# Performance work log

Hardware: AMD Instinct MI355X
Metric: run time of the kernel (lower is better)

The kernel has to match this reference:

```python
import jax, jax.numpy as jnp
import numpy as np
from jax import lax

B, H, W = 8, 64, 64
D_IN, D_OUT, HEADS = 288, 576, 8
WIN, QS = 16, 2
MLP_H, BOT, NEXP = 4 * D_OUT, 32, 2
HEAD_DIM = D_OUT // HEADS


def _ln(x, g, b, eps=1e-6):
    m = jnp.mean(x, axis=-1, keepdims=True)
    v = jnp.var(x, axis=-1, keepdims=True)
    return (x - m) * lax.rsqrt(v + eps) * g + b


def _max_pool2(x):  # NHWC 2x2 max pool, stride 2
    return lax.reduce_window(x, -jnp.inf, lax.max, (1, 2, 2, 1), (1, 2, 2, 1), 'VALID')


def setup_inputs():
    key = jax.random.key(0)
    ks = iter(jax.random.split(key, 16))
    s = 0.02
    p = {}
    p['rgb'] = jax.random.normal(next(ks), (B, H, W, D_IN), jnp.float32)
    p['depth'] = jax.random.normal(next(ks), (B, H, W, D_IN), jnp.float32)
    p['norm1_g'] = jnp.ones((D_IN,), jnp.float32)
    p['norm1_b'] = jnp.zeros((D_IN,), jnp.float32)
    p['proj_w'] = jax.random.normal(next(ks), (D_IN, D_OUT), jnp.float32) * s
    p['proj_b'] = jnp.zeros((D_OUT,), jnp.float32)
    p['qkv_w'] = jax.random.normal(next(ks), (D_IN, 3 * D_OUT), jnp.float32) * s
    p['qkv_b'] = jnp.zeros((3 * D_OUT,), jnp.float32)
    p['attn_proj_w'] = jax.random.normal(next(ks), (D_OUT, D_OUT), jnp.float32) * s
    p['attn_proj_b'] = jnp.zeros((D_OUT,), jnp.float32)
    p['norm2_g'] = jnp.ones((D_OUT,), jnp.float32)
    p['norm2_b'] = jnp.zeros((D_OUT,), jnp.float32)
    p['mlp_w1'] = jax.random.normal(next(ks), (D_OUT, MLP_H), jnp.float32) * s
    p['mlp_b1'] = jnp.zeros((MLP_H,), jnp.float32)
    p['mlp_w2'] = jax.random.normal(next(ks), (MLP_H, D_OUT), jnp.float32) * s
    p['mlp_b2'] = jnp.zeros((D_OUT,), jnp.float32)
    # per-stream (rgb=0, depth=1) MoE adapters: 2 experts, bottleneck 32
    p['ad_gate_w'] = jax.random.normal(next(ks), (2, D_OUT, NEXP), jnp.float32) * s
    p['ad_gate_b'] = jnp.zeros((2, NEXP), jnp.float32)
    p['ad_down_w'] = jax.random.normal(next(ks), (2, NEXP, D_OUT, BOT), jnp.float32) * s
    p['ad_down_b'] = jnp.zeros((2, NEXP, BOT), jnp.float32)
    p['ad_up_w'] = jax.random.normal(next(ks), (2, NEXP, BOT, D_OUT), jnp.float32) * s
    p['ad_up_b'] = jnp.zeros((2, NEXP, D_OUT), jnp.float32)
    return p


def reference(rgb, depth, norm1_g, norm1_b, proj_w, proj_b, qkv_w, qkv_b,
              attn_proj_w, attn_proj_b, norm2_g, norm2_b,
              mlp_w1, mlp_b1, mlp_w2, mlp_b2,
              ad_gate_w, ad_gate_b, ad_down_w, ad_down_b, ad_up_w, ad_up_b):
    nW = H // WIN  # 4 windows per side (64 divisible by 16, no padding)
    w2 = WIN // QS  # pooled window side = 8

    def adapter(x, si):
        gate = jax.nn.softmax(x @ ad_gate_w[si] + ad_gate_b[si], axis=-1)  # [B,h,w,E]
        h = jax.nn.gelu(jnp.einsum('bhwd,edr->bhwer', x, ad_down_w[si]) + ad_down_b[si])
        y = jnp.einsum('bhwer,erd->bhwed', h, ad_up_w[si]) + ad_up_b[si]
        return 0.5 * jnp.sum(gate[..., None] * y, axis=-2)

    def stream(x, si):
        xn = _ln(x, norm1_g, norm1_b)
        # dim changes -> shortcut = do_pool(proj(norm1(x)))
        shortcut = _max_pool2(xn @ proj_w + proj_b)  # [B,32,32,576]
        xw = xn.reshape(B, nW, WIN, nW, WIN, D_IN).transpose(0, 1, 3, 2, 4, 5)
        xw = xw.reshape(B * nW * nW, WIN, WIN, D_IN)
        Bw = xw.shape[0]
        qkv = (xw.reshape(Bw, WIN * WIN, D_IN) @ qkv_w + qkv_b)
        qkv = qkv.reshape(Bw, WIN * WIN, 3, HEADS, HEAD_DIM)
        q, k, v = qkv[:, :, 0], qkv[:, :, 1], qkv[:, :, 2]
        # q-pool (2x2 max) inside each window
        q = _max_pool2(q.reshape(Bw, WIN, WIN, D_OUT)).reshape(Bw, w2 * w2, HEADS, HEAD_DIM)
        scale = 1.0 / np.sqrt(HEAD_DIM).astype(np.float32)
        attn = jax.nn.softmax(jnp.einsum('bqhd,bkhd->bhqk', q, k) * scale, axis=-1)
        o = jnp.einsum('bhqk,bkhd->bqhd', attn, v).reshape(Bw, w2, w2, D_OUT)
        o = o @ attn_proj_w + attn_proj_b
        # unpartition with pooled window size into 32x32
        o = o.reshape(B, nW, nW, w2, w2, D_OUT).transpose(0, 1, 3, 2, 4, 5)
        o = o.reshape(B, nW * w2, nW * w2, D_OUT)
        x = shortcut + o
        h = _ln(x, norm2_g, norm2_b)
        mlp = jax.nn.gelu(h @ mlp_w1 + mlp_b1) @ mlp_w2 + mlp_b2
        return x + mlp + adapter(x, si)

    return jnp.stack([stream(rgb, 0), stream(depth, 1)])  # [2,B,32,32,576]
```

## Files before the change

kernel.cpp:

```cpp
#include <hip/hip_runtime.h>
#include <cstdint>
#include <math.h>
#include <type_traits>

typedef __bf16 bf16_t;
typedef __bf16 bf16x8 __attribute__((ext_vector_type(8)));
typedef float f32x4 __attribute__((ext_vector_type(4)));
typedef uint32_t u32x4 __attribute__((ext_vector_type(4)));
typedef uint32_t u32x2 __attribute__((ext_vector_type(2)));

#define DI __device__ __forceinline__

DI float bflo(uint32_t u){ return __builtin_bit_cast(float, (uint32_t)(u << 16)); }
DI float bfhi(uint32_t u){ return __builtin_bit_cast(float, (uint32_t)(u & 0xffff0000u)); }
DI uint16_t f2bf(float f){ bf16_t h = (bf16_t)f; return __builtin_bit_cast(uint16_t, h); }
DI uint32_t pk2(float a, float b){ return (uint32_t)f2bf(a) | ((uint32_t)f2bf(b) << 16); }
DI float geluf(float x){
  float t = x * x;
  float p = fmaf(t, 0.0356774081f, 0.7978845608f);
  float e = __expf(-2.0f * x * p);
  return x * __builtin_amdgcn_rcpf(1.0f + e);
}

#if defined(__has_builtin)
#if __has_builtin(__builtin_amdgcn_global_load_lds)
#define USE_GLLDS 1
#endif
#endif

#if USE_GLLDS
DI void gload_lds16(const void* g, void* l){
  __builtin_amdgcn_global_load_lds((__attribute__((address_space(1))) void*)g,
                                   (__attribute__((address_space(3))) void*)l, 16, 0, 0);
}
#endif

__global__ __launch_bounds__(256) void vtpad_k(uint16_t* __restrict__ vt)
{
  int idx = blockIdx.x * 256 + threadIdx.x;
  int wh = idx >> 11, r = (idx >> 8) & 7, c = idx & 255;
  vt[((size_t)(wh * 80 + 72 + r)) * 256 + c] = 0;
}

__global__ __launch_bounds__(256) void wtrans_k(const float* __restrict__ W, uint16_t* __restrict__ Wt,
                                                int K, int N, int Np, int ldw, int c0)
{
  int idx = blockIdx.x * 256 + threadIdx.x;
  if (idx >= Np * K) return;
  int n = idx / K, k = idx - n * K;
  float v = (n < N) ? W[(size_t)k * ldw + c0 + n] : 0.0f;
  Wt[idx] = f2bf(v);
}

__global__ __launch_bounds__(256) void mk_m2te_k(const float* __restrict__ w2,
    const float* __restrict__ uw, const float* __restrict__ ub, uint16_t* __restrict__ m2Te)
{
  int idx = blockIdx.x * 256 + threadIdx.x;
  if (idx >= 2 * 640 * 2400) return;
  int si = idx / (640 * 2400);
  int rem = idx - si * 640 * 2400;
  int n = rem / 2400, k = rem - n * 2400;
  float v = 0.0f;
  if (n < 576){
    if (k < 2304) v = w2[(size_t)k * 576 + n];
    else if (k < 2368){
      int e = (k - 2304) >> 5, r = (k - 2304) & 31;
      v = uw[((size_t)(si * 2 + e) * 32 + r) * 576 + n];
    } else if (k < 2370){
      v = ub[(size_t)(si * 2 + (k - 2368)) * 576 + n];
    }
  }
  m2Te[idx] = f2bf(v);
}

__global__ __launch_bounds__(256) void mk_adt_k(const float* __restrict__ dwn, const float* __restrict__ gw,
    const float* __restrict__ dbn, const float* __restrict__ gb,
    uint16_t* __restrict__ adT, float* __restrict__ adB)
{
  int idx = blockIdx.x * 256 + threadIdx.x;
  if (idx >= 2 * 128 * 576) return;
  int si = idx / (128 * 576);
  int rem = idx - si * 128 * 576;
  int n = rem / 576, k = rem - n * 576;
  float v = 0.0f;
  if (n < 64){
    int e = n >> 5, r = n & 31;
    v = dwn[((size_t)(si * 2 + e) * 576 + k) * 32 + r];
  } else if (n < 66){
    v = gw[(size_t)si * 1152 + k * 2 + (n - 64)];
  }
  adT[idx] = f2bf(v);
  if (k == 0){
    float bv = 0.0f;
    if (n < 64) bv = dbn[si * 64 + (n >> 5) * 32 + (n & 31)];
    else if (n < 66) bv = gb[si * 2 + (n - 64)];
    adB[si * 128 + n] = bv;
  }
}

__global__ __launch_bounds__(256) void mk_pqb_k(const float* __restrict__ pb, const float* __restrict__ qb,
                                                float* __restrict__ o)
{
  int i = blockIdx.x * 256 + threadIdx.x;
  if (i < 1152) o[i] = (i < 576) ? pb[i] : qb[i - 576];
}

template<typename TIN>
__global__ __launch_bounds__(256) void ln_k(const TIN* __restrict__ in0, const int D,
                                            const float* __restrict__ g, const float* __restrict__ bb,
                                            uint16_t* __restrict__ outp)
{
  const int token = blockIdx.x * 4 + (threadIdx.x >> 6);
  const int lane = threadIdx.x & 63;
  const TIN* in = in0 + (size_t)token * D;
  const int nf4 = D >> 2;
  f32x4 v[3];
  float s = 0.f, sq = 0.f;
#pragma unroll
  for (int i = 0; i < 3; ++i){
    const int c = lane + 64 * i;
    if (c < nf4){
      if constexpr (std::is_same<TIN, float>::value){
        v[i] = *(const f32x4*)(in + 4 * c);
      } else {
        u32x2 u = *(const u32x2*)((const uint16_t*)in + 4 * c);
        v[i][0] = bflo(u[0]); v[i][1] = bfhi(u[0]);
        v[i][2] = bflo(u[1]); v[i][3] = bfhi(u[1]);
      }
#pragma unroll
      for (int e = 0; e < 4; ++e){ s += v[i][e]; sq += v[i][e] * v[i][e]; }
    }
  }
#pragma unroll
  for (int off = 32; off; off >>= 1){
    s  += __shfl_xor(s, off);
    sq += __shfl_xor(sq, off);
  }
  const float mean = s / (float)D;
  const float var = sq / (float)D - mean * mean;
  const float inv = rsqrtf(var + 1e-6f);
  uint16_t* orow = outp + (size_t)token * D;
#pragma unroll
  for (int i = 0; i < 3; ++i){
    const int c = lane + 64 * i;
    if (c < nf4){
      float f0 = (v[i][0] - mean) * inv * g[4*c+0] + bb[4*c+0];
      float f1 = (v[i][1] - mean) * inv * g[4*c+1] + bb[4*c+1];
      float f2 = (v[i][2] - mean) * inv * g[4*c+2] + bb[4*c+2];
      float f3 = (v[i][3] - mean) * inv * g[4*c+3] + bb[4*c+3];
      u32x2 pk; pk[0] = pk2(f0, f1); pk[1] = pk2(f2, f3);
      *(u32x2*)(orow + 4 * c) = pk;
    }
  }
}

template<int BM>
DI void gemm_core(const uint16_t* __restrict__ A, const uint16_t* __restrict__ Bt,
                  const int K, char* smem, const int tid, f32x4 (*acc)[4])
{
  constexpr int MI = BM / 32;
  constexpr int ABUF = BM * 64;
  char* A0 = smem;
  char* A1 = smem + ABUF;
  char* B0 = smem + 2 * ABUF;
  char* B1 = smem + 2 * ABUF + 8192;
  const int lane = tid & 63;
  const int wid = tid >> 6;
  const int wm = (wid >> 1) * (BM / 2);
  const int wn = (wid & 1) * 64;
  const int r15 = lane & 15, kh = lane >> 4;
  const int rA0 = tid >> 2, c16 = tid & 3;
  const int kS = ((c16 ^ ((rA0 >> 1) & 3)) << 3);

  auto stage = [&](char* Ad, char* Bd, int t){
    const uint16_t* ga0 = A + (size_t)rA0 * K + t * 32 + kS;
    const uint16_t* gb0 = Bt + (size_t)rA0 * K + t * 32 + kS;
    const uint16_t* gb1 = Bt + (size_t)(rA0 + 64) * K + t * 32 + kS;
#if USE_GLLDS
    gload_lds16(ga0, Ad + tid * 16);
    gload_lds16(gb0, Bd + tid * 16);
    gload_lds16(gb1, Bd + tid * 16 + 4096);
    if constexpr (BM == 128){
      const uint16_t* ga1 = A + (size_t)(rA0 + 64) * K + t * 32 + kS;
      gload_lds16(ga1, Ad + tid * 16 + 4096);
    }
#else
    *(u32x4*)(Ad + tid * 16)        = *(const u32x4*)ga0;
    *(u32x4*)(Bd + tid * 16)        = *(const u32x4*)gb0;
    *(u32x4*)(Bd + tid * 16 + 4096) = *(const u32x4*)gb1;
    if constexpr (BM == 128){
      const uint16_t* ga1 = A + (size_t)(rA0 + 64) * K + t * 32 + kS;
      *(u32x4*)(Ad + tid * 16 + 4096) = *(const u32x4*)ga1;
    }
#endif
  };

  stage(A0, B0, 0);
  __syncthreads();
  const int nt = K >> 5;
  for (int t = 0; t < nt; ++t){
    char* Ac = (t & 1) ? A1 : A0;
    char* Bc = (t & 1) ? B1 : B0;
    if (t + 1 < nt) stage((t & 1) ? A0 : A1, (t & 1) ? B0 : B1, t + 1);
    bf16x8 af[MI], bfv[4];
#pragma unroll
    for (int i = 0; i < MI; ++i){
      int rowA = wm + i * 16 + r15;
      af[i] = *(const bf16x8*)(Ac + rowA * 64 + ((kh ^ ((rowA >> 1) & 3)) << 4));
    }
#pragma unroll
    for (int j = 0; j < 4; ++j){
      int rowB = wn + j * 16 + r15;
      bfv[j] = *(const bf16x8*)(Bc + rowB * 64 + ((kh ^ ((rowB >> 1) & 3)) << 4));
    }
#pragma unroll
    for (int i = 0; i < MI; ++i)
#pragma unroll
      for (int j = 0; j < 4; ++j)
        acc[i][j] = __builtin_amdgcn_mfma_f32_16x16x32_bf16(af[i], bfv[j], acc[i][j], 0, 0, 0);
    __syncthreads();
  }
}

__global__ __launch_bounds__(256) void gemm_pkv_k(
    const uint16_t* __restrict__ xn, const uint16_t* __restrict__ pqT, const uint16_t* __restrict__ kvT,
    const float* __restrict__ pqB, const float* __restrict__ kvB,
    uint16_t* __restrict__ sc, uint16_t* __restrict__ qp,
    uint16_t* __restrict__ kb, uint16_t* __restrict__ vt)
{
  __shared__ __align__(16) char smem[34816];
  const int tid = threadIdx.x;
  const int m0 = blockIdx.x * 128;
  const int y = blockIdx.y;
  const bool pool = (y < 9);
  const int n0 = pool ? y * 128 : (y - 9) * 128;
  const uint16_t* Bt = (pool ? pqT : kvT) + (size_t)n0 * 288;
  f32x4 acc[4][4] = {};
  gemm_core<128>(xn + (size_t)m0 * 288, Bt, 288, smem, tid, acc);

  const int lane = tid & 63, wid = tid >> 6;
  const int wm = (wid >> 1) * 64, wn = (wid & 1) * 64;
  const int r15 = lane & 15, kh = lane >> 4;

  if (pool){
    uint16_t* Cp = (uint16_t*)smem;
#pragma unroll
    for (int i = 0; i < 4; ++i)
#pragma unroll
      for (int j = 0; j < 4; ++j)
#pragma unroll
        for (int tt = 0; tt < 4; ++tt){
          int rr2 = wm + i * 16 + kh * 4 + tt;
          int cc = wn + j * 16 + r15;
          Cp[rr2 * 136 + cc] = f2bf(acc[i][j][tt]);
        }
    __syncthreads();
    const int orow0 = m0 >> 2;
#pragma unroll
    for (int e2 = 0; e2 < 16; ++e2){
      int idx = tid + 256 * e2;
      int X = idx >> 7, c = idx & 127;
      int gn = n0 + c;
      float v0 = bflo(Cp[(2 * X) * 136 + c]);
      float v1 = bflo(Cp[(2 * X + 1) * 136 + c]);
      float v2 = bflo(Cp[(64 + 2 * X) * 136 + c]);
      float v3 = bflo(Cp[(65 + 2 * X) * 136 + c]);
      float v = fmaxf(fmaxf(v0, v1), fmaxf(v2, v3)) + pqB[gn];
      if (gn < 576)
        sc[(size_t)(orow0 + X) * 576 + gn] = f2bf(v);
      else
        qp[(size_t)(orow0 + X) * 576 + (gn - 576)] = f2bf(v);
    }
  } else {
    int coln[4]; float bcol[4];
#pragma unroll
    for (int j = 0; j < 4; ++j){
      coln[j] = n0 + wn + j * 16 + r15;
      bcol[j] = kvB[coln[j]];
    }
#pragma unroll
    for (int i = 0; i < 4; ++i)
#pragma unroll
      for (int tt = 0; tt < 4; ++tt){
        const int gm = m0 + wm + i * 16 + kh * 4 + tt;
#pragma unroll
        for (int j = 0; j < 4; ++j){
          float v = acc[i][j][tt] + bcol[j];
          int n = coln[j];
          if (n < 576){
            kb[(size_t)gm * 576 + n] = f2bf(v);
          } else {
            int d = n - 576;
            int hh = d / 72, dd = d - hh * 72;
            int bimg = gm >> 12, yy = (gm >> 6) & 63, xx = gm & 63;
            int w = bimg * 16 + (yy >> 4) * 4 + (xx >> 4);
            int kl = (yy & 15) * 16 + (xx & 15);
            vt[((size_t)(w * 8 + hh) * 80 + dd) * 256 + kl] = f2bf(v);
          }
        }
      }
  }
}

__global__ __launch_bounds__(256) void gemm_add1_k(
    const uint16_t* __restrict__ ob, const uint16_t* __restrict__ aT, const float* __restrict__ bias,
    const uint16_t* __restrict__ sc, uint16_t* __restrict__ x2b)
{
  __shared__ __align__(16) char smem[32768];
  const int tid = threadIdx.x;
  const int m0 = blockIdx.x * 128;
  const int n0 = blockIdx.y * 128;
  f32x4 acc[4][4] = {};
  gemm_core<128>(ob + (size_t)m0 * 576, aT + (size_t)n0 * 576, 576, smem, tid, acc);

  const int lane = tid & 63, wid = tid >> 6;
  const int wm = (wid >> 1) * 64, wn = (wid & 1) * 64;
  const int r15 = lane & 15, kh = lane >> 4;
  int coln[4]; float bcol[4];
#pragma unroll
  for (int j = 0; j < 4; ++j){
    coln[j] = n0 + wn + j * 16 + r15;
    bcol[j] = (coln[j] < 576) ? bias[coln[j]] : 0.0f;
  }
#pragma unroll
  for (int i = 0; i < 4; ++i)
#pragma unroll
    for (int tt = 0; tt < 4; ++tt){
      const int gm = m0 + wm + i * 16 + kh * 4 + tt;
      const size_t ro = (size_t)gm * 576;
#pragma unroll
      for (int j = 0; j < 4; ++j){
        if (coln[j] < 576){
          float v = acc[i][j][tt] + bcol[j] + bflo(sc[ro + coln[j]]);
          x2b[ro + coln[j]] = f2bf(v);
        }
      }
    }
}

__global__ __launch_bounds__(256) void gemm_upad_k(
    const uint16_t* __restrict__ hb, const uint16_t* __restrict__ x2b,
    const uint16_t* __restrict__ m1T, const uint16_t* __restrict__ adT,
    const float* __restrict__ b1, const float* __restrict__ adB,
    uint16_t* __restrict__ mlpA)
{
  __shared__ __align__(16) char smem[32768];
  const int tid = threadIdx.x;
  const int m0 = blockIdx.x * 128;
  const int y = blockIdx.y;
  const bool up = (y < 18);
  const int si = m0 >> 13;
  const int n0 = up ? y * 128 : 0;
  const uint16_t* A = (up ? hb : x2b) + (size_t)m0 * 576;
  const uint16_t* Bt = up ? (m1T + (size_t)n0 * 576) : (adT + (size_t)si * 128 * 576);
  f32x4 acc[4][4] = {};
  gemm_core<128>(A, Bt, 576, smem, tid, acc);

  const int lane = tid & 63, wid = tid >> 6;
  const int wm = (wid >> 1) * 64, wn = (wid & 1) * 64;
  const int r15 = lane & 15, kh = lane >> 4;

  if (up){
#pragma unroll
    for (int i = 0; i < 4; ++i)
#pragma unroll
      for (int tt = 0; tt < 4; ++tt){
        const int gm = m0 + wm + i * 16 + kh * 4 + tt;
#pragma unroll
        for (int j = 0; j < 4; ++j){
          int c = n0 + wn + j * 16 + r15;
          float v = acc[i][j][tt] + b1[c];
          mlpA[(size_t)gm * 2400 + c] = f2bf(geluf(v));
        }
      }
  } else {
    const float* adBp = adB + si * 128;
    float* gl = (float*)smem;
#pragma unroll
    for (int i = 0; i < 4; ++i)
#pragma unroll
      for (int j = 0; j < 4; ++j){
        int c = wn + j * 16 + r15;
        if (c == 64 || c == 65){
#pragma unroll
          for (int tt = 0; tt < 4; ++tt){
            int rr2 = wm + i * 16 + kh * 4 + tt;
            gl[rr2 * 2 + (c - 64)] = acc[i][j][tt] + adBp[c];
          }
        }
      }
    __syncthreads();
#pragma unroll
    for (int i = 0; i < 4; ++i)
#pragma unroll
      for (int tt = 0; tt < 4; ++tt){
        int rr2 = wm + i * 16 + kh * 4 + tt;
        int gm = m0 + rr2;
        float l0 = gl[rr2 * 2], l1 = gl[rr2 * 2 + 1];
        float mx = fmaxf(l0, l1);
        float e0 = __expf(l0 - mx), e1 = __expf(l1 - mx);
        float inv = 0.5f / (e0 + e1);
#pragma unroll
        for (int j = 0; j < 4; ++j){
          int c = wn + j * 16 + r15;
          if (c < 96){
            float val;
            if (c < 64){
              float g = ((c >> 5) == 0 ? e0 : e1) * inv;
              val = g * geluf(acc[i][j][tt] + adBp[c]);
            } else if (c == 64) val = e0 * inv;
            else if (c == 65) val = e1 * inv;
            else val = 0.0f;
            mlpA[(size_t)gm * 2400 + 2304 + c] = f2bf(val);
          }
        }
      }
  }
}

__global__ __launch_bounds__(256) void gemm_addf_k(
    const uint16_t* __restrict__ mlpA, const uint16_t* __restrict__ m2Te, const float* __restrict__ bias,
    const uint16_t* __restrict__ x2b, float* __restrict__ outf)
{
  __shared__ __align__(16) char smem[32768];
  const int tid = threadIdx.x;
  const int m0 = blockIdx.x * 128;
  const int n0 = blockIdx.y * 128;
  const int si = m0 >> 13;
  f32x4 acc[4][4] = {};
  gemm_core<128>(mlpA + (size_t)m0 * 2400, m2Te + (size_t)si * 640 * 2400 + (size_t)n0 * 2400,
                 2400, smem, tid, acc);

  const int lane = tid & 63, wid = tid >> 6;
  const int wm = (wid >> 1) * 64, wn = (wid & 1) * 64;
  const int r15 = lane & 15, kh = lane >> 4;
  int coln[4]; float bcol[4];
#pragma unroll
  for (int j = 0; j < 4; ++j){
    coln[j] = n0 + wn + j * 16 + r15;
    bcol[j] = (coln[j] < 576) ? bias[coln[j]] : 0.0f;
  }
#pragma unroll
  for (int i = 0; i < 4; ++i)
#pragma unroll
    for (int tt = 0; tt < 4; ++tt){
      const int gm = m0 + wm + i * 16 + kh * 4 + tt;
      const size_t ro = (size_t)gm * 576;
#pragma unroll
      for (int j = 0; j < 4; ++j){
        if (coln[j] < 576){
          float v = acc[i][j][tt] + bcol[j] + bflo(x2b[ro + coln[j]]);
          outf[ro + coln[j]] = v;
        }
      }
    }
}

__global__ __launch_bounds__(128) void attn_mfma_k(
    const uint16_t* __restrict__ qp,
    const uint16_t* __restrict__ kb,
    const uint16_t* __restrict__ vt,
    uint16_t* __restrict__ o)
{
  __shared__ float comb[64][88];
  const int tid = threadIdx.x;
  const int wave = tid >> 6;
  const int lane = tid & 63;
  const int r15 = lane & 15;
  const int kh = lane >> 4;
  const int bid = blockIdx.x;
  const int h = bid & 7;
  const int w = bid >> 3;
  const int b = w >> 4;
  const int wy = (w >> 2) & 3;
  const int wx = w & 3;

  const u32x4 ZU = {0, 0, 0, 0};
  const bf16x8 Z8 = __builtin_bit_cast(bf16x8, ZU);
  const float scale = 0.11785113019775793f;

  bf16x8 qf[4][3];
  int qrow[4];
#pragma unroll
  for (int j = 0; j < 4; ++j){
    int q = j * 16 + r15;
    int y = wy * 8 + (q >> 3), x = wx * 8 + (q & 7);
    qrow[j] = b * 1024 + y * 32 + x;
    const uint16_t* qpr = qp + (size_t)qrow[j] * 576 + h * 72;
    qf[j][0] = *(const bf16x8*)(qpr + kh * 8);
    qf[j][1] = *(const bf16x8*)(qpr + 32 + kh * 8);
    qf[j][2] = (kh == 0) ? *(const bf16x8*)(qpr + 64) : Z8;
  }

  float m[4], l[4];
#pragma unroll
  for (int j = 0; j < 4; ++j){ m[j] = -INFINITY; l[j] = 0.0f; }
  f32x4 acco[5][4] = {};
  const size_t vtbase = (size_t)(w * 8 + h) * 80 * 256;

#pragma unroll
  for (int t2 = 0; t2 < 2; ++t2){
    const int t = wave * 2 + t2;
    f32x4 accs[4][4] = {};
#pragma unroll
    for (int i = 0; i < 4; ++i){
      const uint16_t* kr = kb + (size_t)(b * 4096 + (wy * 16 + t * 4 + i) * 64 + wx * 16 + r15) * 576 + h * 72;
      bf16x8 kf0 = *(const bf16x8*)(kr + kh * 8);
      bf16x8 kf1 = *(const bf16x8*)(kr + 32 + kh * 8);
      bf16x8 kf2 = (kh == 0) ? *(const bf16x8*)(kr + 64) : Z8;
#pragma unroll
      for (int j = 0; j < 4; ++j){
        accs[i][j] = __builtin_amdgcn_mfma_f32_16x16x32_bf16(kf0, qf[j][0], accs[i][j], 0, 0, 0);
        accs[i][j] = __builtin_amdgcn_mfma_f32_16x16x32_bf16(kf1, qf[j][1], accs[i][j], 0, 0, 0);
        accs[i][j] = __builtin_amdgcn_mfma_f32_16x16x32_bf16(kf2, qf[j][2], accs[i][j], 0, 0, 0);
      }
    }
#pragma unroll
    for (int j = 0; j < 4; ++j){
      float mx = -INFINITY;
#pragma unroll
      for (int i = 0; i < 4; ++i)
#pragma unroll
        for (int tt = 0; tt < 4; ++tt){
          float sv = accs[i][j][tt] * scale;
          accs[i][j][tt] = sv;
          mx = fmaxf(mx, sv);
        }
      mx = fmaxf(mx, __shfl_xor(mx, 16));
      mx = fmaxf(mx, __shfl_xor(mx, 32));
      float nm = fmaxf(m[j], mx);
      float f = __expf(m[j] - nm);
      m[j] = nm;
      l[j] *= f;
#pragma unroll
      for (int i2 = 0; i2 < 5; ++i2) acco[i2][j] *= f;
      float ls = 0.0f;
#pragma unroll
      for (int i = 0; i < 4; ++i)
#pragma unroll
        for (int tt = 0; tt < 4; ++tt){
          float p = __expf(accs[i][j][tt] - nm);
          accs[i][j][tt] = p;
          ls += p;
        }
      ls += __shfl_xor(ls, 16);
      ls += __shfl_xor(ls, 32);
      l[j] += ls;
    }
    uint32_t pw[4][4][2];
#pragma unroll
    for (int i = 0; i < 4; ++i)
#pragma unroll
      for (int j = 0; j < 4; ++j){
        pw[i][j][0] = pk2(accs[i][j][0], accs[i][j][1]);
        pw[i][j][1] = pk2(accs[i][j][2], accs[i][j][3]);
      }
#pragma unroll
    for (int ks = 0; ks < 2; ++ks){
      bf16x8 pb[4];
#pragma unroll
      for (int j = 0; j < 4; ++j){
        u32x4 u = {pw[2 * ks][j][0], pw[2 * ks][j][1], pw[2 * ks + 1][j][0], pw[2 * ks + 1][j][1]};
        pb[j] = __builtin_bit_cast(bf16x8, u);
      }
#pragma unroll
      for (int i2 = 0; i2 < 5; ++i2){
        const uint16_t* vr = vt + vtbase + (size_t)(i2 * 16 + r15) * 256 + t * 64 + ks * 32 + kh * 4;
        u32x2 lo = *(const u32x2*)(vr);
        u32x2 hi = *(const u32x2*)(vr + 16);
        u32x4 av = {lo[0], lo[1], hi[0], hi[1]};
        bf16x8 va = __builtin_bit_cast(bf16x8, av);
#pragma unroll
        for (int j = 0; j < 4; ++j)
          acco[i2][j] = __builtin_amdgcn_mfma_f32_16x16x32_bf16(va, pb[j], acco[i2][j], 0, 0, 0);
      }
    }
  }

  if (wave == 1){
#pragma unroll
    for (int j = 0; j < 4; ++j){ comb[lane][j] = m[j]; comb[lane][4 + j] = l[j]; }
#pragma unroll
    for (int i2 = 0; i2 < 5; ++i2)
#pragma unroll
      for (int j = 0; j < 4; ++j)
#pragma unroll
        for (int tt = 0; tt < 4; ++tt)
          comb[lane][8 + (i2 * 4 + j) * 4 + tt] = acco[i2][j][tt];
  }
  __syncthreads();
  if (wave == 0){
    float fs0[4], fs1[4];
#pragma unroll
    for (int j = 0; j < 4; ++j){
      float m1v = comb[lane][j], l1v = comb[lane][4 + j];
      float nm = fmaxf(m[j], m1v);
      fs0[j] = __expf(m[j] - nm);
      fs1[j] = __expf(m1v - nm);
      l[j] = l[j] * fs0[j] + l1v * fs1[j];
    }
#pragma unroll
    for (int j = 0; j < 4; ++j){
      float inv = 1.0f / l[j];
      uint16_t* orow = o + (size_t)qrow[j] * 576 + h * 72;
#pragma unroll
      for (int i2 = 0; i2 < 5; ++i2)
#pragma unroll
        for (int tt = 0; tt < 4; ++tt){
          int d = i2 * 16 + kh * 4 + tt;
          if (d < 72){
            float ov = acco[i2][j][tt] * fs0[j] + comb[lane][8 + (i2 * 4 + j) * 4 + tt] * fs1[j];
            orow[d] = f2bf(ov * inv);
          }
        }
    }
  }
}

extern "C" void kernel_launch(void* const* d_in, const int* in_sizes, int n_in,
                              void* d_out, int out_size, void* d_ws, size_t ws_size,
                              hipStream_t stream)
{
  (void)in_sizes; (void)n_in; (void)out_size; (void)ws_size;
  const float* srcs[2] = { (const float*)d_in[0], (const float*)d_in[1] };
  const float* n1g    = (const float*)d_in[2];
  const float* n1b    = (const float*)d_in[3];
  const float* proj_w = (const float*)d_in[4];
  const float* proj_b = (const float*)d_in[5];
  const float* qkv_w  = (const float*)d_in[6];
  const float* qkv_b  = (const float*)d_in[7];
  const float* ap_w   = (const float*)d_in[8];
  const float* ap_b   = (const float*)d_in[9];
  const float* n2g    = (const float*)d_in[10];
  const float* n2b    = (const float*)d_in[11];
  const float* w1     = (const float*)d_in[12];
  const float* b1     = (const float*)d_in[13];
  const float* w2     = (const float*)d_in[14];
  const float* b2     = (const float*)d_in[15];
  const float* gw     = (const float*)d_in[16];
  const float* gb     = (const float*)d_in[17];
  const float* dwn    = (const float*)d_in[18];
  const float* dbn    = (const float*)d_in[19];
  const float* uw     = (const float*)d_in[20];
  const float* ub     = (const float*)d_in[21];

  char* ws = (char*)d_ws;
  size_t off = 0;
  auto alloc = [&](size_t bytes){ size_t o = off; off += (bytes + 255) & ~(size_t)255; return o; };

  uint16_t* pqT   = (uint16_t*)(ws + alloc((size_t)1152 * 288 * 2));
  float*    pqB   = (float*)(ws + alloc((size_t)1152 * 4));
  uint16_t* kvT   = (uint16_t*)(ws + alloc((size_t)1152 * 288 * 2));
  uint16_t* aT    = (uint16_t*)(ws + alloc((size_t)640 * 576 * 2));
  uint16_t* m1T   = (uint16_t*)(ws + alloc((size_t)2304 * 576 * 2));
  uint16_t* m2Te  = (uint16_t*)(ws + alloc((size_t)2 * 640 * 2400 * 2));
  uint16_t* adT   = (uint16_t*)(ws + alloc((size_t)2 * 128 * 576 * 2));
  float*    adB   = (float*)(ws + alloc((size_t)2 * 128 * 4));
  uint16_t* xn   = (uint16_t*)(ws + alloc((size_t)32768 * 288 * 2));
  uint16_t* sc2  = (uint16_t*)(ws + alloc((size_t)16384 * 576 * 2));
  size_t oQP = alloc((size_t)16384 * 576 * 2);
  uint16_t* qp2  = (uint16_t*)(ws + oQP);
  uint16_t* x2b  = (uint16_t*)(ws + oQP);
  uint16_t* kb   = (uint16_t*)(ws + alloc((size_t)32768 * 576 * 2));
  size_t oVT = alloc((size_t)16384 * 2400 * 2);
  uint16_t* vt   = (uint16_t*)(ws + oVT);
  uint16_t* mlpA = (uint16_t*)(ws + oVT);
  size_t oOB = alloc((size_t)16384 * 576 * 2);
  uint16_t* ob2  = (uint16_t*)(ws + oOB);
  uint16_t* hb2  = (uint16_t*)(ws + oOB);

  wtrans_k<<<(576 * 288 + 255) / 256, 256, 0, stream>>>(proj_w, pqT, 288, 576, 576, 576, 0);
  wtrans_k<<<(576 * 288 + 255) / 256, 256, 0, stream>>>(qkv_w, pqT + (size_t)576 * 288, 288, 576, 576, 1728, 0);
  mk_pqb_k<<<5, 256, 0, stream>>>(proj_b, qkv_b, pqB);
  wtrans_k<<<(1152 * 288 + 255) / 256, 256, 0, stream>>>(qkv_w, kvT, 288, 1152, 1152, 1728, 576);
  wtrans_k<<<(640 * 576 + 255) / 256, 256, 0, stream>>>(ap_w, aT, 576, 576, 640, 576, 0);
  wtrans_k<<<(2304 * 576 + 255) / 256, 256, 0, stream>>>(w1, m1T, 576, 2304, 2304, 2304, 0);
  mk_m2te_k<<<(2 * 640 * 2400 + 255) / 256, 256, 0, stream>>>(w2, uw, ub, m2Te);
  mk_adt_k<<<(2 * 128 * 576 + 255) / 256, 256, 0, stream>>>(dwn, gw, dbn, gb, adT, adB);

  for (int si = 0; si < 2; ++si){
    const size_t half = (size_t)si * 8192 * 576;

    ln_k<float><<<8192, 256, 0, stream>>>(srcs[si], 288, n1g, n1b, xn);

    vtpad_k<<<(1024 * 8 * 256) / 256, 256, 0, stream>>>(vt);

    gemm_pkv_k<<<dim3(256, 18), 256, 0, stream>>>(xn, pqT, kvT, pqB, qkv_b + 576,
                                                  sc2 + half, qp2 + half, kb, vt);

    attn_mfma_k<<<1024, 128, 0, stream>>>(qp2 + half, kb, vt, ob2 + half);
  }

  gemm_add1_k<<<dim3(128, 5), 256, 0, stream>>>(ob2, aT, ap_b, sc2, x2b);

  ln_k<uint16_t><<<4096, 256, 0, stream>>>(x2b, 576, n2g, n2b, hb2);

  gemm_upad_k<<<dim3(128, 19), 256, 0, stream>>>(hb2, x2b, m1T, adT, b1, adB, mlpA);

  gemm_addf_k<<<dim3(128, 5), 256, 0, stream>>>(mlpA, m2Te, b2, x2b, (float*)d_out);
}
```

Baseline: 565.6 us.

## Enlarge pool/KV GEMM M-tile to 256 rows and pool directly in registers

The fused projection/Q-pool/KV GEMM now processes 256 rows per block instead of 128, halving the grid. Each warp's 128-row slice covers two full image rows, so the 2x2 max pool can be taken straight from accumulator registers (acc[i] vs acc[i+4]) instead of staging through shared memory. This removes the LDS round-trip, a barrier and repeated B-tile loads, but doubles accumulator registers and raises shared memory use, which may cut occupancy.

Measured after the change: 610.2 us. +7.9%, slower.

```diff
diff --git a/kernel.cpp b/kernel.cpp
--- a/kernel.cpp
+++ b/kernel.cpp
@@ -159,6 +159,7 @@
                   const int K, char* smem, const int tid, f32x4 (*acc)[4])
 {
   constexpr int MI = BM / 32;
+  constexpr int NSA = BM / 64;
   constexpr int ABUF = BM * 64;
   char* A0 = smem;
   char* A1 = smem + ABUF;
@@ -173,25 +174,23 @@
   const int kS = ((c16 ^ ((rA0 >> 1) & 3)) << 3);
 
   auto stage = [&](char* Ad, char* Bd, int t){
-    const uint16_t* ga0 = A + (size_t)rA0 * K + t * 32 + kS;
+#pragma unroll
+    for (int s = 0; s < NSA; ++s){
+      const uint16_t* ga = A + (size_t)(rA0 + 64 * s) * K + t * 32 + kS;
+#if USE_GLLDS
+      gload_lds16(ga, Ad + tid * 16 + s * 4096);
+#else
+      *(u32x4*)(Ad + tid * 16 + s * 4096) = *(const u32x4*)ga;
+#endif
+    }
     const uint16_t* gb0 = Bt + (size_t)rA0 * K + t * 32 + kS;
     const uint16_t* gb1 = Bt + (size_t)(rA0 + 64) * K + t * 32 + kS;
 #if USE_GLLDS
-    gload_lds16(ga0, Ad + tid * 16);
     gload_lds16(gb0, Bd + tid * 16);
     gload_lds16(gb1, Bd + tid * 16 + 4096);
-    if constexpr (BM == 128){
-      const uint16_t* ga1 = A + (size_t)(rA0 + 64) * K + t * 32 + kS;
-      gload_lds16(ga1, Ad + tid * 16 + 4096);
-    }
 #else
-    *(u32x4*)(Ad + tid * 16)        = *(const u32x4*)ga0;
     *(u32x4*)(Bd + tid * 16)        = *(const u32x4*)gb0;
     *(u32x4*)(Bd + tid * 16 + 4096) = *(const u32x4*)gb1;
-    if constexpr (BM == 128){
-      const uint16_t* ga1 = A + (size_t)(rA0 + 64) * K + t * 32 + kS;
-      *(u32x4*)(Ad + tid * 16 + 4096) = *(const u32x4*)ga1;
-    }
 #endif
   };
 
@@ -228,58 +227,48 @@
     uint16_t* __restrict__ sc, uint16_t* __restrict__ qp,
     uint16_t* __restrict__ kb, uint16_t* __restrict__ vt)
 {
-  __shared__ __align__(16) char smem[34816];
+  __shared__ __align__(16) char smem[49152];
   const int tid = threadIdx.x;
-  const int m0 = blockIdx.x * 128;
+  const int m0 = blockIdx.x * 256;
   const int y = blockIdx.y;
   const bool pool = (y < 9);
   const int n0 = pool ? y * 128 : (y - 9) * 128;
   const uint16_t* Bt = (pool ? pqT : kvT) + (size_t)n0 * 288;
-  f32x4 acc[4][4] = {};
-  gemm_core<128>(xn + (size_t)m0 * 288, Bt, 288, smem, tid, acc);
+  f32x4 acc[8][4] = {};
+  gemm_core<256>(xn + (size_t)m0 * 288, Bt, 288, smem, tid, acc);
 
   const int lane = tid & 63, wid = tid >> 6;
-  const int wm = (wid >> 1) * 64, wn = (wid & 1) * 64;
+  const int wm = (wid >> 1) * 128, wn = (wid & 1) * 64;
   const int r15 = lane & 15, kh = lane >> 4;
+  int coln[4];
+#pragma unroll
+  for (int j = 0; j < 4; ++j) coln[j] = n0 + wn + j * 16 + r15;
 
   if (pool){
-    uint16_t* Cp = (uint16_t*)smem;
+    const int prow0 = ((m0 + wm) >> 7) * 32;
+    float bcol[4];
+#pragma unroll
+    for (int j = 0; j < 4; ++j) bcol[j] = pqB[coln[j]];
 #pragma unroll
     for (int i = 0; i < 4; ++i)
 #pragma unroll
-      for (int j = 0; j < 4; ++j)
-#pragma unroll
-        for (int tt = 0; tt < 4; ++tt){
-          int rr2 = wm + i * 16 + kh * 4 + tt;
-          int cc = wn + j * 16 + r15;
-          Cp[rr2 * 136 + cc] = f2bf(acc[i][j][tt]);
-        }
-    __syncthreads();
-    const int orow0 = m0 >> 2;
-#pragma unroll
-    for (int e2 = 0; e2 < 16; ++e2){
-      int idx = tid + 256 * e2;
-      int X = idx >> 7, c = idx & 127;
-      int gn = n0 + c;
-      float v0 = bflo(Cp[(2 * X) * 136 + c]);
-      float v1 = bflo(Cp[(2 * X + 1) * 136 + c]);
-      float v2 = bflo(Cp[(64 + 2 * X) * 136 + c]);
-      float v3 = bflo(Cp[(65 + 2 * X) * 136 + c]);
-      float v = fmaxf(fmaxf(v0, v1), fmaxf(v2, v3)) + pqB[gn];
-      if (gn < 576)
-        sc[(size_t)(orow0 + X) * 576 + gn] = f2bf(v);
-      else
-        qp[(size_t)(orow0 + X) * 576 + (gn - 576)] = f2bf(v);
-    }
+      for (int tth = 0; tth < 2; ++tth){
+        const int prow = prow0 + i * 8 + kh * 2 + tth;
+        const size_t ro = (size_t)prow * 576;
+#pragma unroll
+        for (int j = 0; j < 4; ++j){
+          float v = fmaxf(fmaxf(acc[i][j][2 * tth], acc[i][j][2 * tth + 1]),
+                          fmaxf(acc[i + 4][j][2 * tth], acc[i + 4][j][2 * tth + 1])) + bcol[j];
+          if (coln[j] < 576) sc[ro + coln[j]] = f2bf(v);
+          else               qp[ro + coln[j] - 576] = f2bf(v);
+        }
+      }
   } else {
-    int coln[4]; float bcol[4];
-#pragma unroll
-    for (int j = 0; j < 4; ++j){
-      coln[j] = n0 + wn + j * 16 + r15;
-      bcol[j] = kvB[coln[j]];
-    }
-#pragma unroll
-    for (int i = 0; i < 4; ++i)
+    float bcol[4];
+#pragma unroll
+    for (int j = 0; j < 4; ++j) bcol[j] = kvB[coln[j]];
+#pragma unroll
+    for (int i = 0; i < 8; ++i)
 #pragma unroll
       for (int tt = 0; tt < 4; ++tt){
         const int gm = m0 + wm + i * 16 + kh * 4 + tt;
@@ -685,7 +674,7 @@
 
     vtpad_k<<<(1024 * 8 * 256) / 256, 256, 0, stream>>>(vt);
 
-    gemm_pkv_k<<<dim3(256, 18), 256, 0, stream>>>(xn, pqT, kvT, pqB, qkv_b + 576,
+    gemm_pkv_k<<<dim3(128, 18), 256, 0, stream>>>(xn, pqT, kvT, pqB, qkv_b + 576,
                                                   sc2 + half, qp2 + half, kb, vt);
 
     attn_mfma_k<<<1024, 128, 0, stream>>>(qp2 + half, kb, vt, ob2 + half);
```
